# Optimization experiments

Hardware: AMD Instinct MI355X
Metric: run time of the kernel (lower is better)

## Reference

```python
import jax, jax.numpy as jnp
import numpy as np

B, T, DM = 2, 4096, 2048
H, HKV, HD, CHUNK = 16, 4, 128, 128
N_REP = H // HKV


def setup_inputs() -> dict:
    key = jax.random.key(0)
    ks = jax.random.split(key, 5)
    s = 0.02
    return {
        "x": jax.random.normal(ks[0], (B, T, DM), jnp.float32),
        "wq": jax.random.normal(ks[1], (DM, H * HD), jnp.float32) * s,
        "wk": jax.random.normal(ks[2], (DM, HKV * HD), jnp.float32) * s,
        "wv": jax.random.normal(ks[3], (DM, HKV * HD), jnp.float32) * s,
        "wo": jax.random.normal(ks[4], (H * HD, DM), jnp.float32) * s,
    }


def _chunked_attention(q, k, v):
    # q,k,v: (B,H,T,D); causal online-softmax over K/V chunks of size CHUNK
    b, h, tq, d = q.shape
    tk = k.shape[2]
    n_chunks = tk // CHUNK
    scale = 1.0 / np.sqrt(d).astype(np.float32)
    k_chunks = k.reshape(b, h, n_chunks, CHUNK, d).transpose(2, 0, 1, 3, 4)
    v_chunks = v.reshape(b, h, n_chunks, CHUNK, d).transpose(2, 0, 1, 3, 4)
    starts = (jnp.arange(n_chunks) * CHUNK).astype(jnp.int32)
    q_pos = jnp.arange(tq)[:, None]  # (Tq,1)

    def step(carry, xs):
        m, s, o = carry  # (b,h,tq), (b,h,tq), (b,h,tq,d)
        kc, vc, st = xs
        scores = scale * jnp.einsum('bhqd,bhkd->bhqk', q, kc)
        k_pos = st + jnp.arange(CHUNK)[None, :]  # (1,CHUNK)
        mask = k_pos > q_pos  # (tq,CHUNK) True = masked
        scores = jnp.where(mask[None, None], -jnp.inf, scores)
        chunk_max = scores.max(axis=-1)
        new_max = jnp.maximum(m, chunk_max)
        exp_new = jnp.exp(scores - new_max[..., None])
        chunk_sum = exp_new.sum(axis=-1)
        scale_prev = jnp.exp(m - new_max)
        new_sum = scale_prev * s + chunk_sum
        new_out = scale_prev[..., None] * o + jnp.einsum('bhqk,bhkd->bhqd', exp_new, vc)
        return (new_max, new_sum, new_out), None

    init = (
        jnp.full((b, h, tq), -jnp.inf, jnp.float32),
        jnp.zeros((b, h, tq), jnp.float32),
        jnp.zeros((b, h, tq, d), jnp.float32),
    )
    (m, s, o), _ = jax.lax.scan(step, init, (k_chunks, v_chunks, starts))
    return o / s[..., None]


def reference(x, wq, wk, wv, wo):
    b, t, _ = x.shape
    q = (x @ wq).reshape(b, t, H, HD)
    k = (x @ wk).reshape(b, t, HKV, HD)
    v = (x @ wv).reshape(b, t, HKV, HD)
    # GQA expansion: each kv head repeated N_REP times along head axis
    k = jnp.repeat(k, N_REP, axis=2)
    v = jnp.repeat(v, N_REP, axis=2)
    q = q.transpose(0, 2, 1, 3)  # (B,H,T,D)
    k = k.transpose(0, 2, 1, 3)
    v = v.transpose(0, 2, 1, 3)
    out = _chunked_attention(q, k, v)
    out = out.transpose(0, 2, 1, 3).reshape(b, t, H * HD)
    return out @ wo
```

## Files before the change

### kernel.cpp

```cpp
#include <hip/hip_runtime.h>

typedef unsigned short u16;
typedef __attribute__((ext_vector_type(4))) float f32x4;
typedef __attribute__((ext_vector_type(16))) float f32x16;
typedef __attribute__((ext_vector_type(8))) short bf16x8;

#define GLOBAL_AS(p) ((__attribute__((address_space(1))) void*)(void*)(p))
#define LDS_AS(p)    ((__attribute__((address_space(3))) void*)(p))

__device__ inline u16 f2bf(float f) {
    union { float f; unsigned int u; } v; v.f = f;
    unsigned int u = v.u;
    unsigned int r = (u + 0x7fffu + ((u >> 16) & 1u)) >> 16;
    return (u16)r;
}
__device__ inline unsigned cvt_pk2(float lo, float hi) {
    unsigned r;
    asm("v_cvt_pk_bf16_f32 %0, %1, %2" : "=v"(r) : "v"(lo), "v"(hi));
    return r;
}

__global__ void cvt_kernel(const float* __restrict__ in, u16* __restrict__ out, int n4) {
    int i = blockIdx.x * blockDim.x + threadIdx.x;
    int stride = gridDim.x * blockDim.x;
    for (int idx = i; idx < n4; idx += stride) {
        float4 v = ((const float4*)in)[idx];
        ushort4 o;
        o.x = f2bf(v.x); o.y = f2bf(v.y); o.z = f2bf(v.z); o.w = f2bf(v.w);
        ((ushort4*)out)[idx] = o;
    }
}

__global__ void tcvt_kernel(const float* __restrict__ w, u16* __restrict__ wt, int N) {
    __shared__ float tile[64][65];
    int t = threadIdx.x;
    int tx = t & 63, ty = t >> 6;
    int k0 = blockIdx.y * 64, n0 = blockIdx.x * 64;
#pragma unroll
    for (int i = 0; i < 16; ++i)
        tile[ty * 16 + i][tx] = w[(size_t)(k0 + ty * 16 + i) * N + n0 + tx];
    __syncthreads();
#pragma unroll
    for (int i = 0; i < 16; ++i)
        wt[(size_t)(n0 + ty * 16 + i) * 2048 + k0 + tx] = f2bf(tile[tx][ty * 16 + i]);
}

template<bool C_F32, bool C_T>
__global__ __launch_bounds__(256, 3) void gemm_kernel(const u16* __restrict__ A,
                                                      const u16* __restrict__ Bt,
                                                      void* __restrict__ Cv, int ldc,
                                                      float cscale) {
    __shared__ __align__(16) u16 As[128 * 32];
    __shared__ __align__(16) u16 Bs[128 * 32];
    int tid = threadIdx.x;
    int lane = tid & 63, wid = tid >> 6;
    int lr = lane & 15, lg = lane >> 4;
    int wr = wid >> 1, wc = wid & 1;
    int l = blockIdx.x + 4 * blockIdx.y;
    int s = (l & 7) * 32 + (l >> 3);
    size_t m0 = (size_t)(s >> 2) * 128, n0 = (size_t)(s & 3) * 128;

    int srow = wid * 16 + (lane >> 2);
    int cbs = ((lane & 3) * 16) ^ ((srow & 3) << 4);
    const u16* Ar = A + (m0 + srow) * 2048 + (cbs >> 1);
    const u16* Br = Bt + (n0 + srow) * 2048 + (cbs >> 1);
    u16* lA0 = &As[(wid * 16) * 32];
    u16* lA1 = &As[(64 + wid * 16) * 32];
    u16* lB0 = &Bs[(wid * 16) * 32];
    u16* lB1 = &Bs[(64 + wid * 16) * 32];

    int fco = (((lg * 16) ^ ((lr & 3) << 4)) >> 1);

    f32x4 acc[4][4] = {};

    for (int k0 = 0; k0 < 2048; k0 += 32) {
        __builtin_amdgcn_global_load_lds(GLOBAL_AS(Ar + k0), LDS_AS(lA0), 16, 0, 0);
        __builtin_amdgcn_global_load_lds(GLOBAL_AS(Ar + (size_t)64 * 2048 + k0), LDS_AS(lA1), 16, 0, 0);
        __builtin_amdgcn_global_load_lds(GLOBAL_AS(Br + k0), LDS_AS(lB0), 16, 0, 0);
        __builtin_amdgcn_global_load_lds(GLOBAL_AS(Br + (size_t)64 * 2048 + k0), LDS_AS(lB1), 16, 0, 0);
        __syncthreads();

        bf16x8 af[4], bfr[4];
#pragma unroll
        for (int m = 0; m < 4; ++m) af[m] = *(const bf16x8*)&As[(wr * 64 + m * 16 + lr) * 32 + fco];
#pragma unroll
        for (int n = 0; n < 4; ++n) bfr[n] = *(const bf16x8*)&Bs[(wc * 64 + n * 16 + lr) * 32 + fco];
#pragma unroll
        for (int m = 0; m < 4; ++m)
#pragma unroll
            for (int n = 0; n < 4; ++n)
                acc[m][n] = __builtin_amdgcn_mfma_f32_16x16x32_bf16(af[m], bfr[n], acc[m][n], 0, 0, 0);
        __syncthreads();
    }

#pragma unroll
    for (int m = 0; m < 4; ++m)
#pragma unroll
        for (int n = 0; n < 4; ++n)
#pragma unroll
            for (int i = 0; i < 4; ++i) {
                size_t row = m0 + wr * 64 + m * 16 + lg * 4 + i;
                size_t col = n0 + wc * 64 + n * 16 + lr;
                float v = acc[m][n][i] * cscale;
                size_t off = C_T ? (col * (size_t)ldc + row) : (row * (size_t)ldc + col);
                if (C_F32) ((float*)Cv)[off] = v;
                else       ((u16*)Cv)[off] = f2bf(v);
            }
}

template<bool C_F32>
__global__ __launch_bounds__(512, 2) void gemm256_kernel(const u16* __restrict__ A,
                                                         const u16* __restrict__ Bt,
                                                         void* __restrict__ Cv, int ldc,
                                                         float cscale) {
    __shared__ __align__(16) u16 As[2][256 * 64];
    __shared__ __align__(16) u16 Bs[2][256 * 64];
    int tid = threadIdx.x;
    int lane = tid & 63, wid = tid >> 6;
    int lr = lane & 15, lg = lane >> 4;
    int wm = wid >> 2, wn = wid & 3;
    int l = blockIdx.x + 8 * blockIdx.y;
    int s = (l & 7) * 32 + (l >> 3);
    size_t m0 = (size_t)(s >> 3) * 256, n0 = (size_t)(s & 7) * 256;

    int srow = tid >> 3;
    int scb = ((tid & 7) * 16) ^ ((srow & 7) << 4);
    const u16* Ag = A + (m0 + srow) * 2048 + (scb >> 1);
    const u16* Bg = Bt + (n0 + srow) * 2048 + (scb >> 1);
    int lbase = (wid * 8) * 64;

    int fc0 = ((0 * 64 + lg * 16) ^ ((lr & 7) << 4)) >> 1;
    int fc1 = ((1 * 64 + lg * 16) ^ ((lr & 7) << 4)) >> 1;

    f32x4 acc[8][4] = {};

#define STAGE256(buf, kt)                                                                   \
    do {                                                                                     \
        int kof = (kt) * 64;                                                                 \
        _Pragma("unroll")                                                                    \
        for (int r = 0; r < 4; ++r) {                                                        \
            __builtin_amdgcn_global_load_lds(GLOBAL_AS(Ag + (size_t)r * 64 * 2048 + kof),    \
                                             LDS_AS(&As[buf][lbase + r * 64 * 64]), 16, 0, 0); \
            __builtin_amdgcn_global_load_lds(GLOBAL_AS(Bg + (size_t)r * 64 * 2048 + kof),    \
                                             LDS_AS(&Bs[buf][lbase + r * 64 * 64]), 16, 0, 0); \
        }                                                                                    \
    } while (0)

    STAGE256(0, 0);
    for (int t = 0; t < 32; ++t) {
        int buf = t & 1;
        if (t + 1 < 32) {
            STAGE256(buf ^ 1, t + 1);
            asm volatile("s_waitcnt vmcnt(8)" ::: "memory");
        } else {
            asm volatile("s_waitcnt vmcnt(0)" ::: "memory");
        }
        __builtin_amdgcn_s_barrier();

        __builtin_amdgcn_s_setprio(1);
#pragma unroll
        for (int ks = 0; ks < 2; ++ks) {
            int fc = ks ? fc1 : fc0;
            bf16x8 bfrg[4];
#pragma unroll
            for (int n = 0; n < 4; ++n)
                bfrg[n] = *(const bf16x8*)&Bs[buf][(wn * 64 + n * 16 + lr) * 64 + fc];
            bf16x8 afrg[8];
#pragma unroll
            for (int m = 0; m < 8; ++m)
                afrg[m] = *(const bf16x8*)&As[buf][(wm * 128 + m * 16 + lr) * 64 + fc];
#pragma unroll
            for (int m = 0; m < 8; ++m)
#pragma unroll
                for (int n = 0; n < 4; ++n)
                    acc[m][n] = __builtin_amdgcn_mfma_f32_16x16x32_bf16(afrg[m], bfrg[n], acc[m][n], 0, 0, 0);
        }
        __builtin_amdgcn_s_setprio(0);

        asm volatile("s_waitcnt lgkmcnt(0)" ::: "memory");
        __builtin_amdgcn_s_barrier();
    }
#undef STAGE256

#pragma unroll
    for (int m = 0; m < 8; ++m)
#pragma unroll
        for (int n = 0; n < 4; ++n)
#pragma unroll
            for (int i = 0; i < 4; ++i) {
                size_t row = m0 + wm * 128 + m * 16 + lg * 4 + i;
                size_t col = n0 + wn * 64 + n * 16 + lr;
                float v = acc[m][n][i] * cscale;
                size_t off = row * (size_t)ldc + col;
                if (C_F32) ((float*)Cv)[off] = v;
                else       ((u16*)Cv)[off] = f2bf(v);
            }
}

__global__ __launch_bounds__(256, 2) void attn_kernel(const u16* __restrict__ Q,
                                                      const u16* __restrict__ K,
                                                      const u16* __restrict__ Vt,
                                                      u16* __restrict__ O) {
    __shared__ __align__(16) u16 Ks[2][64 * 128];
    __shared__ __align__(16) u16 Vs[2][128 * 64];
    int tid = threadIdx.x;
    int lane = tid & 63, w = tid >> 6;
    int q5 = lane & 31, h = lane >> 5;
    int bid = blockIdx.x;
    int swz = (bid & 7) * 64 + (bid >> 3);
    int bx = swz & 15;
    int bh = swz >> 4;
    int b = bh >> 4, hh = bh & 15, hkv = hh >> 2;

    const u16* kp = K + (size_t)(b * 4096) * 512 + hkv * 128;
    const u16* vp = Vt + (size_t)(hkv * 128) * 8192 + (size_t)b * 4096;

    int kRb = 16 * w + (lane >> 4);
    int kcb = (lane & 15) * 16;
    int vRb = 32 * w + (lane >> 3);
    int vcb = (lane & 7) * 16;

    auto stage = [&](int buf, int kv) {
#pragma unroll
        for (int q = 0; q < 4; ++q) {
            int R = kRb + 4 * q;
            int cb = kcb ^ ((R & 15) << 4);
            const u16* gp = kp + (size_t)(kv + R) * 512 + (cb >> 1);
            u16* lp = &Ks[buf][(16 * w + 4 * q) * 128];
            __builtin_amdgcn_global_load_lds(GLOBAL_AS(gp), LDS_AS(lp), 16, 0, 0);
        }
#pragma unroll
        for (int q = 0; q < 4; ++q) {
            int R = vRb + 8 * q;
            int cb = vcb ^ ((R & 7) << 4);
            const u16* gp = vp + (size_t)R * 8192 + kv + (cb >> 1);
            u16* lp = &Vs[buf][(32 * w + 8 * q) * 64];
            __builtin_amdgcn_global_load_lds(GLOBAL_AS(gp), LDS_AS(lp), 16, 0, 0);
        }
    };

    const float FMAX = 20.0f;

    for (int half = 0; half < 2; ++half) {
        int qt = half ? (31 - bx) : bx;
        int q0 = qt * 128;
        int nc = 2 * qt + 2;
        int qb0 = q0 + w * 32;

        const u16* qp = Q + (size_t)(b * 4096 + qb0 + q5) * 2048 + hh * 128;
        bf16x8 qf[8];
#pragma unroll
        for (int dk = 0; dk < 8; ++dk)
            qf[dk] = *(const bf16x8*)(qp + dk * 16 + h * 8);

        float s_ = 0.f;
        f32x16 oaccT[4] = {};

        stage(0, 0);
        asm volatile("s_waitcnt vmcnt(0)" ::: "memory");
        __syncthreads();

        int cur = 0;
        for (int c = 0; c < nc; ++c) {
            int kv0 = c * 64;
            if (c + 1 < nc) stage(cur ^ 1, kv0 + 64);

            if (kv0 <= qb0 + 31) {
                bool act1 = (kv0 + 32 <= qb0 + 31);
                f32x16 s0acc = {}, s1acc = {};
                __builtin_amdgcn_s_setprio(1);
#pragma unroll
                for (int dk = 0; dk < 8; ++dk) {
                    int cb = (dk * 32 + h * 16) ^ ((q5 & 15) << 4);
                    bf16x8 k0 = *(const bf16x8*)&Ks[cur][q5 * 128 + (cb >> 1)];
                    s0acc = __builtin_amdgcn_mfma_f32_32x32x16_bf16(k0, qf[dk], s0acc, 0, 0, 0);
                }
                if (act1) {
#pragma unroll
                    for (int dk = 0; dk < 8; ++dk) {
                        int cb = (dk * 32 + h * 16) ^ ((q5 & 15) << 4);
                        bf16x8 k1 = *(const bf16x8*)&Ks[cur][(32 + q5) * 128 + (cb >> 1)];
                        s1acc = __builtin_amdgcn_mfma_f32_32x32x16_bf16(k1, qf[dk], s1acc, 0, 0, 0);
                    }
                }
                __builtin_amdgcn_s_setprio(0);

                bool need_mask = (kv0 + 63 > qb0);
                int qrel = qb0 + q5 - kv0;
                float pe0[16], pe1[16];
                float rs = 0.f;
                if (need_mask) {
#pragma unroll
                    for (int r = 0; r < 16; ++r) {
                        int ki = (r & 3) + 8 * (r >> 2) + 4 * h;
                        float v = (ki > qrel) ? -1e30f : s0acc[r];
                        float e = __builtin_amdgcn_exp2f(v - FMAX);
                        pe0[r] = e; rs += e;
                    }
                } else {
#pragma unroll
                    for (int r = 0; r < 16; ++r) {
                        float e = __builtin_amdgcn_exp2f(s0acc[r] - FMAX);
                        pe0[r] = e; rs += e;
                    }
                }
                if (act1) {
                    if (need_mask) {
#pragma unroll
                        for (int r = 0; r < 16; ++r) {
                            int ki = 32 + (r & 3) + 8 * (r >> 2) + 4 * h;
                            float v = (ki > qrel) ? -1e30f : s1acc[r];
                            float e = __builtin_amdgcn_exp2f(v - FMAX);
                            pe1[r] = e; rs += e;
                        }
                    } else {
#pragma unroll
                        for (int r = 0; r < 16; ++r) {
                            float e = __builtin_amdgcn_exp2f(s1acc[r] - FMAX);
                            pe1[r] = e; rs += e;
                        }
                    }
                }
                {
                    union { float f; int i; } ri; ri.f = rs;
#if __has_builtin(__builtin_amdgcn_permlane32_swap)
                    auto rr = __builtin_amdgcn_permlane32_swap(ri.i, ri.i, false, false);
                    union { int i; float f; } a0, a1; a0.i = rr[0]; a1.i = rr[1];
                    rs = a0.f + a1.f;
#else
                    rs += __shfl_xor(rs, 32);
#endif
                }
                s_ += rs;

                unsigned Wf[8][2];
#pragma unroll
                for (int j = 0; j < 4; ++j) {
                    Wf[j][0] = cvt_pk2(pe0[4 * j], pe0[4 * j + 1]);
                    Wf[j][1] = cvt_pk2(pe0[4 * j + 2], pe0[4 * j + 3]);
                }
                if (act1) {
#pragma unroll
                    for (int j = 0; j < 4; ++j) {
                        Wf[4 + j][0] = cvt_pk2(pe1[4 * j], pe1[4 * j + 1]);
                        Wf[4 + j][1] = cvt_pk2(pe1[4 * j + 2], pe1[4 * j + 3]);
                    }
                } else {
#pragma unroll
                    for (int j = 0; j < 4; ++j) { Wf[4 + j][0] = 0; Wf[4 + j][1] = 0; }
                }

                __builtin_amdgcn_s_setprio(1);
#pragma unroll
                for (int t = 0; t < 4; ++t) {
                    union { unsigned u[4]; bf16x8 v; } pb;
#if __has_builtin(__builtin_amdgcn_permlane32_swap)
                    {
                        auto r0 = __builtin_amdgcn_permlane32_swap((int)Wf[2 * t][0], (int)Wf[2 * t + 1][0], false, false);
                        auto r1 = __builtin_amdgcn_permlane32_swap((int)Wf[2 * t][1], (int)Wf[2 * t + 1][1], false, false);
                        pb.u[0] = (unsigned)r0[0];
                        pb.u[1] = (unsigned)r1[0];
                        pb.u[2] = (unsigned)r0[1];
                        pb.u[3] = (unsigned)r1[1];
                    }
#else
                    {
                        unsigned send0 = h ? Wf[2 * t][0] : Wf[2 * t + 1][0];
                        unsigned send1 = h ? Wf[2 * t][1] : Wf[2 * t + 1][1];
                        unsigned recv0 = (unsigned)__shfl_xor((int)send0, 32);
                        unsigned recv1 = (unsigned)__shfl_xor((int)send1, 32);
                        unsigned own0 = h ? Wf[2 * t + 1][0] : Wf[2 * t][0];
                        unsigned own1 = h ? Wf[2 * t + 1][1] : Wf[2 * t][1];
                        pb.u[0] = h ? recv0 : own0;
                        pb.u[1] = h ? recv1 : own1;
                        pb.u[2] = h ? own0 : recv0;
                        pb.u[3] = h ? own1 : recv1;
                    }
#endif
                    int cb = (t * 32 + h * 16) ^ ((q5 & 7) << 4);
#pragma unroll
                    for (int ob = 0; ob < 4; ++ob) {
                        bf16x8 vA = *(const bf16x8*)&Vs[cur][(ob * 32 + q5) * 64 + (cb >> 1)];
                        oaccT[ob] = __builtin_amdgcn_mfma_f32_32x32x16_bf16(vA, pb.v, oaccT[ob], 0, 0, 0);
                    }
                }
                __builtin_amdgcn_s_setprio(0);
            }

            asm volatile("s_waitcnt vmcnt(0)" ::: "memory");
            __syncthreads();
            cur ^= 1;
        }

        u16* op = O + (size_t)(b * 4096 + qb0 + q5) * 2048 + hh * 128;
        float inv = 1.0f / s_;
#pragma unroll
        for (int ob = 0; ob < 4; ++ob)
#pragma unroll
            for (int j = 0; j < 4; ++j) {
                uint2 st2;
                st2.x = cvt_pk2(oaccT[ob][4 * j] * inv, oaccT[ob][4 * j + 1] * inv);
                st2.y = cvt_pk2(oaccT[ob][4 * j + 2] * inv, oaccT[ob][4 * j + 3] * inv);
                *(uint2*)(op + ob * 32 + 8 * j + 4 * h) = st2;
            }
    }
}

extern "C" void kernel_launch(void* const* d_in, const int* in_sizes, int n_in,
                              void* d_out, int out_size, void* d_ws, size_t ws_size,
                              hipStream_t stream) {
    const float* x  = (const float*)d_in[0];
    const float* wq = (const float*)d_in[1];
    const float* wk = (const float*)d_in[2];
    const float* wv = (const float*)d_in[3];
    const float* wo = (const float*)d_in[4];
    float* out = (float*)d_out;
    u16* ws = (u16*)d_ws;

    u16* XB  = ws;
    u16* WQT = ws + 16777216;
    u16* WKT = WQT + 4194304;
    u16* WVT = WKT + 1048576;
    u16* WOT = WVT + 1048576;
    u16* QB  = WOT + 4194304;
    u16* KB  = QB + 16777216;
    u16* VT  = KB + 4194304;
    u16* ATTN = XB;

    const float SCALE_LOG2E = 0.12751744f;

    cvt_kernel<<<2048, 256, 0, stream>>>(x, XB, 16777216 / 4);
    tcvt_kernel<<<dim3(32, 32), 256, 0, stream>>>(wq, WQT, 2048);
    tcvt_kernel<<<dim3(8, 32), 256, 0, stream>>>(wk, WKT, 512);
    tcvt_kernel<<<dim3(8, 32), 256, 0, stream>>>(wv, WVT, 512);
    tcvt_kernel<<<dim3(32, 32), 256, 0, stream>>>(wo, WOT, 2048);

    gemm256_kernel<false><<<dim3(8, 32), 512, 0, stream>>>(XB, WQT, (void*)QB, 2048, SCALE_LOG2E);
    gemm_kernel<false, false><<<dim3(4, 64), 256, 0, stream>>>(XB, WKT, (void*)KB, 512, 1.0f);
    gemm_kernel<false, true ><<<dim3(4, 64), 256, 0, stream>>>(XB, WVT, (void*)VT, 8192, 1.0f);

    attn_kernel<<<512, 256, 0, stream>>>(QB, KB, VT, ATTN);

    gemm256_kernel<true><<<dim3(8, 32), 512, 0, stream>>>(ATTN, WOT, (void*)out, 2048, 1.0f);
}
```

Before: 419.5 us.

## Software-pipeline QK^T one chunk ahead with triple-buffered K tiles

```diff
diff --git a/kernel.cpp b/kernel.cpp
--- a/kernel.cpp
+++ b/kernel.cpp
@@ -201,7 +201,7 @@
                                                       const u16* __restrict__ K,
                                                       const u16* __restrict__ Vt,
                                                       u16* __restrict__ O) {
-    __shared__ __align__(16) u16 Ks[2][64 * 128];
+    __shared__ __align__(16) u16 Ks[3][64 * 128];
     __shared__ __align__(16) u16 Vs[2][128 * 64];
     int tid = threadIdx.x;
     int lane = tid & 63, w = tid >> 6;
@@ -220,7 +220,7 @@
     int vRb = 32 * w + (lane >> 3);
     int vcb = (lane & 7) * 16;
 
-    auto stage = [&](int buf, int kv) {
+    auto stageK = [&](int buf, int kv) {
 #pragma unroll
         for (int q = 0; q < 4; ++q) {
             int R = kRb + 4 * q;
@@ -229,6 +229,8 @@
             u16* lp = &Ks[buf][(16 * w + 4 * q) * 128];
             __builtin_amdgcn_global_load_lds(GLOBAL_AS(gp), LDS_AS(lp), 16, 0, 0);
         }
+    };
+    auto stageV = [&](int buf, int kv) {
 #pragma unroll
         for (int q = 0; q < 4; ++q) {
             int R = vRb + 8 * q;
@@ -239,8 +241,6 @@
         }
     };
 
-    const float FMAX = 20.0f;
-
     for (int half = 0; half < 2; ++half) {
         int qt = half ? (31 - bx) : bx;
         int q0 = qt * 128;
@@ -256,140 +256,166 @@
         float s_ = 0.f;
         f32x16 oaccT[4] = {};
 
-        stage(0, 0);
+        auto qk = [&](int slot, f32x16& sa0, f32x16& sa1, bool a0, bool a1) {
+            if (!a0) return;
+            f32x16 z = {};
+            sa0 = z;
+#pragma unroll
+            for (int dk = 0; dk < 8; ++dk) {
+                int cb = (dk * 32 + h * 16) ^ ((q5 & 15) << 4);
+                bf16x8 k0 = *(const bf16x8*)&Ks[slot][q5 * 128 + (cb >> 1)];
+                sa0 = __builtin_amdgcn_mfma_f32_32x32x16_bf16(k0, qf[dk], sa0, 0, 0, 0);
+            }
+            if (a1) {
+                sa1 = z;
+#pragma unroll
+                for (int dk = 0; dk < 8; ++dk) {
+                    int cb = (dk * 32 + h * 16) ^ ((q5 & 15) << 4);
+                    bf16x8 k1 = *(const bf16x8*)&Ks[slot][(32 + q5) * 128 + (cb >> 1)];
+                    sa1 = __builtin_amdgcn_mfma_f32_32x32x16_bf16(k1, qf[dk], sa1, 0, 0, 0);
+                }
+            }
+        };
+
+        auto smpv = [&](int c, f32x16& sc0, f32x16& sc1) {
+            int kv0 = c * 64;
+            if (kv0 > qb0 + 31) return;
+            bool act1 = (kv0 + 32 <= qb0 + 31);
+            bool need_mask = (kv0 + 63 > qb0);
+            int qrel = qb0 + q5 - kv0;
+            float pe0[16], pe1[16];
+            float rs = 0.f;
+            if (need_mask) {
+#pragma unroll
+                for (int r = 0; r < 16; ++r) {
+                    int ki = (r & 3) + 8 * (r >> 2) + 4 * h;
+                    float v = (ki > qrel) ? -1e30f : sc0[r];
+                    float e = __builtin_amdgcn_exp2f(v);
+                    pe0[r] = e; rs += e;
+                }
+            } else {
+#pragma unroll
+                for (int r = 0; r < 16; ++r) {
+                    float e = __builtin_amdgcn_exp2f(sc0[r]);
+                    pe0[r] = e; rs += e;
+                }
+            }
+            if (act1) {
+                if (need_mask) {
+#pragma unroll
+                    for (int r = 0; r < 16; ++r) {
+                        int ki = 32 + (r & 3) + 8 * (r >> 2) + 4 * h;
+                        float v = (ki > qrel) ? -1e30f : sc1[r];
+                        float e = __builtin_amdgcn_exp2f(v);
+                        pe1[r] = e; rs += e;
+                    }
+                } else {
+#pragma unroll
+                    for (int r = 0; r < 16; ++r) {
+                        float e = __builtin_amdgcn_exp2f(sc1[r]);
+                        pe1[r] = e; rs += e;
+                    }
+                }
+            }
+            {
+                union { float f; int i; } ri; ri.f = rs;
+#if __has_builtin(__builtin_amdgcn_permlane32_swap)
+                auto rr = __builtin_amdgcn_permlane32_swap(ri.i, ri.i, false, false);
+                union { int i; float f; } a0, a1; a0.i = rr[0]; a1.i = rr[1];
+                rs = a0.f + a1.f;
+#else
+                rs += __shfl_xor(rs, 32);
+#endif
+            }
+            s_ += rs;
+
+            unsigned Wf[8][2];
+#pragma unroll
+            for (int j = 0; j < 4; ++j) {
+                Wf[j][0] = cvt_pk2(pe0[4 * j], pe0[4 * j + 1]);
+                Wf[j][1] = cvt_pk2(pe0[4 * j + 2], pe0[4 * j + 3]);
+            }
+            if (act1) {
+#pragma unroll
+                for (int j = 0; j < 4; ++j) {
+                    Wf[4 + j][0] = cvt_pk2(pe1[4 * j], pe1[4 * j + 1]);
+                    Wf[4 + j][1] = cvt_pk2(pe1[4 * j + 2], pe1[4 * j + 3]);
+                }
+            } else {
+#pragma unroll
+                for (int j = 0; j < 4; ++j) { Wf[4 + j][0] = 0; Wf[4 + j][1] = 0; }
+            }
+
+            int vslot = c & 1;
+            __builtin_amdgcn_s_setprio(1);
+#pragma unroll
+            for (int t = 0; t < 4; ++t) {
+                union { unsigned u[4]; bf16x8 v; } pb;
+#if __has_builtin(__builtin_amdgcn_permlane32_swap)
+                {
+                    auto r0 = __builtin_amdgcn_permlane32_swap((int)Wf[2 * t][0], (int)Wf[2 * t + 1][0], false, false);
+                    auto r1 = __builtin_amdgcn_permlane32_swap((int)Wf[2 * t][1], (int)Wf[2 * t + 1][1], false, false);
+                    pb.u[0] = (unsigned)r0[0];
+                    pb.u[1] = (unsigned)r1[0];
+                    pb.u[2] = (unsigned)r0[1];
+                    pb.u[3] = (unsigned)r1[1];
+                }
+#else
+                {
+                    unsigned send0 = h ? Wf[2 * t][0] : Wf[2 * t + 1][0];
+                    unsigned send1 = h ? Wf[2 * t][1] : Wf[2 * t + 1][1];
+                    unsigned recv0 = (unsigned)__shfl_xor((int)send0, 32);
+                    unsigned recv1 = (unsigned)__shfl_xor((int)send1, 32);
+                    unsigned own0 = h ? Wf[2 * t + 1][0] : Wf[2 * t][0];
+                    unsigned own1 = h ? Wf[2 * t + 1][1] : Wf[2 * t][1];
+                    pb.u[0] = h ? recv0 : own0;
+                    pb.u[1] = h ? recv1 : own1;
+                    pb.u[2] = h ? own0 : recv0;
+                    pb.u[3] = h ? own1 : recv1;
+                }
+#endif
+                int cb = (t * 32 + h * 16) ^ ((q5 & 7) << 4);
+#pragma unroll
+                for (int ob = 0; ob < 4; ++ob) {
+                    bf16x8 vA = *(const bf16x8*)&Vs[vslot][(ob * 32 + q5) * 64 + (cb >> 1)];
+                    oaccT[ob] = __builtin_amdgcn_mfma_f32_32x32x16_bf16(vA, pb.v, oaccT[ob], 0, 0, 0);
+                }
+            }
+            __builtin_amdgcn_s_setprio(0);
+        };
+
+        auto iter = [&](int cc, f32x16& sc0, f32x16& sc1, f32x16& sn0, f32x16& sn1) {
+            if (cc + 2 < nc) {
+                stageK((cc + 2) % 3, (cc + 2) * 64);
+                stageV((cc + 1) & 1, (cc + 1) * 64);
+                asm volatile("s_waitcnt vmcnt(8)" ::: "memory");
+            } else if (cc + 1 < nc) {
+                stageV((cc + 1) & 1, (cc + 1) * 64);
+                asm volatile("s_waitcnt vmcnt(4)" ::: "memory");
+            } else {
+                asm volatile("s_waitcnt vmcnt(0)" ::: "memory");
+            }
+            __syncthreads();
+            if (cc + 1 < nc) {
+                int kvn = (cc + 1) * 64;
+                qk((cc + 1) % 3, sn0, sn1, kvn <= qb0 + 31, kvn + 32 <= qb0 + 31);
+            }
+            smpv(cc, sc0, sc1);
+            __syncthreads();
+        };
+
+        stageK(0, 0);
+        stageK(1, 64);
+        stageV(0, 0);
         asm volatile("s_waitcnt vmcnt(0)" ::: "memory");
         __syncthreads();
 
-        int cur = 0;
-        for (int c = 0; c < nc; ++c) {
-            int kv0 = c * 64;
-            if (c + 1 < nc) stage(cur ^ 1, kv0 + 64);
-
-            if (kv0 <= qb0 + 31) {
-                bool act1 = (kv0 + 32 <= qb0 + 31);
-                f32x16 s0acc = {}, s1acc = {};
-                __builtin_amdgcn_s_setprio(1);
-#pragma unroll
-                for (int dk = 0; dk < 8; ++dk) {
-                    int cb = (dk * 32 + h * 16) ^ ((q5 & 15) << 4);
-                    bf16x8 k0 = *(const bf16x8*)&Ks[cur][q5 * 128 + (cb >> 1)];
-                    s0acc = __builtin_amdgcn_mfma_f32_32x32x16_bf16(k0, qf[dk], s0acc, 0, 0, 0);
-                }
-                if (act1) {
-#pragma unroll
-                    for (int dk = 0; dk < 8; ++dk) {
-                        int cb = (dk * 32 + h * 16) ^ ((q5 & 15) << 4);
-                        bf16x8 k1 = *(const bf16x8*)&Ks[cur][(32 + q5) * 128 + (cb >> 1)];
-                        s1acc = __builtin_amdgcn_mfma_f32_32x32x16_bf16(k1, qf[dk], s1acc, 0, 0, 0);
-                    }
-                }
-                __builtin_amdgcn_s_setprio(0);
-
-                bool need_mask = (kv0 + 63 > qb0);
-                int qrel = qb0 + q5 - kv0;
-                float pe0[16], pe1[16];
-                float rs = 0.f;
-                if (need_mask) {
-#pragma unroll
-                    for (int r = 0; r < 16; ++r) {
-                        int ki = (r & 3) + 8 * (r >> 2) + 4 * h;
-                        float v = (ki > qrel) ? -1e30f : s0acc[r];
-                        float e = __builtin_amdgcn_exp2f(v - FMAX);
-                        pe0[r] = e; rs += e;
-                    }
-                } else {
-#pragma unroll
-                    for (int r = 0; r < 16; ++r) {
-                        float e = __builtin_amdgcn_exp2f(s0acc[r] - FMAX);
-                        pe0[r] = e; rs += e;
-                    }
-                }
-                if (act1) {
-                    if (need_mask) {
-#pragma unroll
-                        for (int r = 0; r < 16; ++r) {
-                            int ki = 32 + (r & 3) + 8 * (r >> 2) + 4 * h;
-                            float v = (ki > qrel) ? -1e30f : s1acc[r];
-                            float e = __builtin_amdgcn_exp2f(v - FMAX);
-                            pe1[r] = e; rs += e;
-                        }
-                    } else {
-#pragma unroll
-                        for (int r = 0; r < 16; ++r) {
-                            float e = __builtin_amdgcn_exp2f(s1acc[r] - FMAX);
-                            pe1[r] = e; rs += e;
-                        }
-                    }
-                }
-                {
-                    union { float f; int i; } ri; ri.f = rs;
-#if __has_builtin(__builtin_amdgcn_permlane32_swap)
-                    auto rr = __builtin_amdgcn_permlane32_swap(ri.i, ri.i, false, false);
-                    union { int i; float f; } a0, a1; a0.i = rr[0]; a1.i = rr[1];
-                    rs = a0.f + a1.f;
-#else
-                    rs += __shfl_xor(rs, 32);
-#endif
-                }
-                s_ += rs;
-
-                unsigned Wf[8][2];
-#pragma unroll
-                for (int j = 0; j < 4; ++j) {
-                    Wf[j][0] = cvt_pk2(pe0[4 * j], pe0[4 * j + 1]);
-                    Wf[j][1] = cvt_pk2(pe0[4 * j + 2], pe0[4 * j + 3]);
-                }
-                if (act1) {
-#pragma unroll
-                    for (int j = 0; j < 4; ++j) {
-                        Wf[4 + j][0] = cvt_pk2(pe1[4 * j], pe1[4 * j + 1]);
-                        Wf[4 + j][1] = cvt_pk2(pe1[4 * j + 2], pe1[4 * j + 3]);
-                    }
-                } else {
-#pragma unroll
-                    for (int j = 0; j < 4; ++j) { Wf[4 + j][0] = 0; Wf[4 + j][1] = 0; }
-                }
-
-                __builtin_amdgcn_s_setprio(1);
-#pragma unroll
-                for (int t = 0; t < 4; ++t) {
-                    union { unsigned u[4]; bf16x8 v; } pb;
-#if __has_builtin(__builtin_amdgcn_permlane32_swap)
-                    {
-                        auto r0 = __builtin_amdgcn_permlane32_swap((int)Wf[2 * t][0], (int)Wf[2 * t + 1][0], false, false);
-                        auto r1 = __builtin_amdgcn_permlane32_swap((int)Wf[2 * t][1], (int)Wf[2 * t + 1][1], false, false);
-                        pb.u[0] = (unsigned)r0[0];
-                        pb.u[1] = (unsigned)r1[0];
-                        pb.u[2] = (unsigned)r0[1];
-                        pb.u[3] = (unsigned)r1[1];
-                    }
-#else
-                    {
-                        unsigned send0 = h ? Wf[2 * t][0] : Wf[2 * t + 1][0];
-                        unsigned send1 = h ? Wf[2 * t][1] : Wf[2 * t + 1][1];
-                        unsigned recv0 = (unsigned)__shfl_xor((int)send0, 32);
-                        unsigned recv1 = (unsigned)__shfl_xor((int)send1, 32);
-                        unsigned own0 = h ? Wf[2 * t + 1][0] : Wf[2 * t][0];
-                        unsigned own1 = h ? Wf[2 * t + 1][1] : Wf[2 * t][1];
-                        pb.u[0] = h ? recv0 : own0;
-                        pb.u[1] = h ? recv1 : own1;
-                        pb.u[2] = h ? own0 : recv0;
-                        pb.u[3] = h ? own1 : recv1;
-                    }
-#endif
-                    int cb = (t * 32 + h * 16) ^ ((q5 & 7) << 4);
-#pragma unroll
-                    for (int ob = 0; ob < 4; ++ob) {
-                        bf16x8 vA = *(const bf16x8*)&Vs[cur][(ob * 32 + q5) * 64 + (cb >> 1)];
-                        oaccT[ob] = __builtin_amdgcn_mfma_f32_32x32x16_bf16(vA, pb.v, oaccT[ob], 0, 0, 0);
-                    }
-                }
-                __builtin_amdgcn_s_setprio(0);
-            }
-
-            asm volatile("s_waitcnt vmcnt(0)" ::: "memory");
-            __syncthreads();
-            cur ^= 1;
+        f32x16 sA0 = {}, sA1 = {}, sB0 = {}, sB1 = {};
+        qk(0, sA0, sA1, true, 32 <= qb0 + 31);
+
+        for (int c = 0; c < nc; c += 2) {
+            iter(c, sA0, sA1, sB0, sB1);
+            iter(c + 1, sB0, sB1, sA0, sA1);
         }
 
         u16* op = O + (size_t)(b * 4096 + qb0 + q5) * 2048 + hh * 128;
```

Measured after the change: 418.9 us. No clear change (-0.1%).
